# Kernel optimization log

Hardware: AMD Instinct MI355X
Metric: run time of the kernel (lower is better)

Reference implementation:

```python
import jax, jax.numpy as jnp
import numpy as np

B, S, H = 16, 512, 768
T, HD = 9, 64  # num_entity_types, head_size
MASK_VAL = 1e12


def setup_inputs() -> dict:
    key = jax.random.key(0)
    k1, k2 = jax.random.split(key)
    hidden_states = jax.random.normal(k1, (B, S, H), dtype=jnp.float32)
    attention_mask = jnp.ones((B, S), dtype=jnp.int32)
    W_dense = jax.random.normal(k2, (H, T * HD * 2), dtype=jnp.float32) * (H ** -0.5)
    b_dense = jnp.zeros((T * HD * 2,), dtype=jnp.float32)
    return {"hidden_states": hidden_states, "attention_mask": attention_mask,
            "W_dense": W_dense, "b_dense": b_dense}


def _rope_rotate(x, cos_pos, sin_pos):
    # x: [B, S, T, HD]; rotate interleaved pairs
    x2 = jnp.stack([-x[..., 1::2], x[..., ::2]], axis=-1).reshape(x.shape)
    return x * cos_pos + x2 * sin_pos


def reference(hidden_states, attention_mask, W_dense, b_dense):
    b, s, _ = hidden_states.shape
    out = hidden_states @ W_dense + b_dense              # [B,S,T*HD*2]
    out = out.reshape(b, s, T, HD, 2)
    qw, kw = out[..., 0], out[..., 1]                    # [B,S,T,HD]

    # sinusoidal RoPE angles
    pos = jnp.arange(s, dtype=jnp.float32)               # [S]
    inv_freq = jnp.power(10000.0, -2.0 * jnp.arange(HD // 2, dtype=jnp.float32) / HD)
    ang = pos[:, None] * inv_freq[None, :]               # [S, HD/2]
    cos_pos = jnp.repeat(jnp.cos(ang), 2, axis=-1)[None, :, None, :]  # [1,S,1,HD]
    sin_pos = jnp.repeat(jnp.sin(ang), 2, axis=-1)[None, :, None, :]

    qw = _rope_rotate(qw, cos_pos, sin_pos)
    kw = _rope_rotate(kw, cos_pos, sin_pos)

    # biaffine scores: [B,T,S,S]
    logits = jnp.einsum('bmtd,bntd->btmn', qw, kw) / (HD ** 0.5)

    am = attention_mask.astype(logits.dtype)
    pad_mask = (am[:, :, None] * am[:, None, :])[:, None, :, :]  # [B,1,S,S]
    logits = logits - (1.0 - pad_mask) * MASK_VAL

    triu = jnp.triu(jnp.ones((s, s), dtype=logits.dtype), k=0)
    logits = logits - (1.0 - triu) * MASK_VAL
    return logits
```

## Files before the change

### kernel.cpp

```cpp
#include <hip/hip_runtime.h>

#define B_  16
#define S_  512
#define H_  768
#define T_  9
#define HD_ 64
#define N1  (T_*HD_*2)
#define M1  (B_*S_)
#define NT1 (H_/32)

typedef __attribute__((ext_vector_type(8))) short bf16x8;
typedef __attribute__((ext_vector_type(4))) float f32x4;

#define GLB(p) ((const __attribute__((address_space(1))) void*)(p))
#define LDSP(p) ((__attribute__((address_space(3))) void*)(p))

__device__ inline unsigned short f2bf(float f){
  union { float f; unsigned u; } v; v.f = f;
  unsigned r = v.u + 0x7fffu + ((v.u >> 16) & 1u);
  return (unsigned short)(r >> 16);
}

__global__ __launch_bounds__(256) void prep_all(
    const float* __restrict__ hs, short* __restrict__ Abf,
    const float* __restrict__ W, short* __restrict__ Wt,
    float2* __restrict__ tab)
{
  __shared__ float tile[32][33];
  const int bx = blockIdx.x, tid = threadIdx.x;
  if(bx < 3072){
    int i = bx*2048 + tid*8;
    float4 a0 = *(const float4*)(hs + i);
    float4 a1 = *(const float4*)(hs + i + 4);
    bf16x8 r;
    r[0]=f2bf(a0.x); r[1]=f2bf(a0.y); r[2]=f2bf(a0.z); r[3]=f2bf(a0.w);
    r[4]=f2bf(a1.x); r[5]=f2bf(a1.y); r[6]=f2bf(a1.z); r[7]=f2bf(a1.w);
    *(bf16x8*)(Abf + i) = r;
  } else if(bx < 3936){
    int idx = bx - 3072;
    int n0 = (idx % 36)*32, k0 = (idx / 36)*32;
    int tx = tid & 31, ty = tid >> 5;
    #pragma unroll
    for(int r = 0; r < 32; r += 8)
      tile[ty + r][tx] = W[(size_t)(k0 + ty + r)*N1 + n0 + tx];
    __syncthreads();
    #pragma unroll
    for(int r = 0; r < 32; r += 8)
      Wt[(size_t)(n0 + ty + r)*H_ + k0 + tx] = f2bf(tile[tx][ty + r]);
  } else {
    int i = (bx - 3936)*256 + tid;
    int s = i >> 5, p = i & 31;
    float inv = powf(10000.f, -2.f*(float)p/64.f);
    float a = (float)s * inv;
    tab[i] = make_float2(cosf(a), sinf(a));
  }
}

__global__ __launch_bounds__(256) void gemm1_rope(
    const short* __restrict__ Abf, const short* __restrict__ Wt,
    const float* __restrict__ bias, const float2* __restrict__ tab,
    short* __restrict__ Qr, short* __restrict__ Kr)
{
  __shared__ short As[2][128*32];
  __shared__ short Bs[2][128*32];
  const int tid  = threadIdx.x;
  const int lane = tid & 63, w = tid >> 6;
  const int wm = (w >> 1) * 64, wn = (w & 1) * 64;
  const int m0 = blockIdx.x * 128, n0 = blockIdx.y * 128;
  const int lr = lane & 15, lk = (lane >> 4) * 8;

  const int sr = tid >> 2;
  const int sc = (tid & 3) * 8;
  const short* aS = Abf + (size_t)(m0 + sr) * H_ + sc;
  const short* bS = Wt  + (size_t)(n0 + sr) * H_ + sc;
  const int dOff = tid * 8;

#define STAGE1(buf, k0) do{ \
    __builtin_amdgcn_global_load_lds(GLB(aS + (k0)),         LDSP(&As[buf][dOff]),        16, 0, 0); \
    __builtin_amdgcn_global_load_lds(GLB(aS + 64*H_ + (k0)), LDSP(&As[buf][dOff + 2048]), 16, 0, 0); \
    __builtin_amdgcn_global_load_lds(GLB(bS + (k0)),         LDSP(&Bs[buf][dOff]),        16, 0, 0); \
    __builtin_amdgcn_global_load_lds(GLB(bS + 64*H_ + (k0)), LDSP(&Bs[buf][dOff + 2048]), 16, 0, 0); \
  }while(0)

  f32x4 acc[4][4] = {};
  STAGE1(0, 0);

  for(int it = 0; it < NT1; ++it){
    __syncthreads();
    const int cur = it & 1;
    if(it + 1 < NT1) STAGE1(cur ^ 1, (it + 1) * 32);

    bf16x8 aF[4], bF[4];
    #pragma unroll
    for(int i = 0; i < 4; ++i) aF[i] = *(const bf16x8*)(&As[cur][(wm + i*16 + lr)*32 + lk]);
    #pragma unroll
    for(int j = 0; j < 4; ++j) bF[j] = *(const bf16x8*)(&Bs[cur][(wn + j*16 + lr)*32 + lk]);
    #pragma unroll
    for(int i = 0; i < 4; ++i)
      #pragma unroll
      for(int j = 0; j < 4; ++j)
        acc[i][j] = __builtin_amdgcn_mfma_f32_16x16x32_bf16(bF[j], aF[i], acc[i][j], 0, 0, 0);
  }

  const int t = n0 >> 7;
  #pragma unroll
  for(int i = 0; i < 4; ++i){
    int m  = m0 + wm + i*16 + lr;
    int bi = m >> 9, sp = m & 511;
    size_t rowoff = ((size_t)(bi*T_ + t)*S_ + sp)*HD_;
    #pragma unroll
    for(int j = 0; j < 4; ++j){
      int nq  = n0 + wn + j*16 + ((lane >> 4) << 2);
      int hd0 = (nq >> 1) & 63;
      int p   = (nq >> 2) & 31;
      float4 bv = *(const float4*)(bias + nq);
      float2 cs = tab[sp*32 + p];
      float q0 = acc[i][j][0] + bv.x;
      float k0v= acc[i][j][1] + bv.y;
      float q1 = acc[i][j][2] + bv.z;
      float k1v= acc[i][j][3] + bv.w;
      float rq0 = q0*cs.x - q1*cs.y, rq1 = q1*cs.x + q0*cs.y;
      float rk0 = k0v*cs.x - k1v*cs.y, rk1 = k1v*cs.x + k0v*cs.y;
      unsigned uq = (unsigned)f2bf(rq0) | ((unsigned)f2bf(rq1) << 16);
      unsigned uk = (unsigned)f2bf(rk0) | ((unsigned)f2bf(rk1) << 16);
      *(unsigned*)(Qr + rowoff + hd0) = uq;
      *(unsigned*)(Kr + rowoff + hd0) = uk;
    }
  }
}

__global__ __launch_bounds__(256) void gemm2_mask(
    const short* __restrict__ Qr, const short* __restrict__ Kr,
    const int* __restrict__ am, float* __restrict__ out)
{
  const int lane = threadIdx.x & 63;
  const int w    = threadIdx.x >> 6;
  const int bt   = blockIdx.z;
  const int b    = bt / T_;
  const int n0   = blockIdx.x * 128 + (w & 1) * 64;
  const int m0   = blockIdx.y * 128 + (w >> 1) * 64;
  const int lr   = lane & 15;
  const int lk   = (lane >> 4) * 8;

  const short* Q = Qr + (size_t)bt * S_ * HD_;
  const short* K = Kr + (size_t)bt * S_ * HD_;
  f32x4 acc[4][4] = {};

  #pragma unroll
  for(int ks = 0; ks < HD_; ks += 32){
    bf16x8 aF[4], bF[4];
    #pragma unroll
    for(int i = 0; i < 4; ++i) aF[i] = *(const bf16x8*)(Q + (size_t)(m0 + i*16 + lr)*HD_ + ks + lk);
    #pragma unroll
    for(int j = 0; j < 4; ++j) bF[j] = *(const bf16x8*)(K + (size_t)(n0 + j*16 + lr)*HD_ + ks + lk);
    #pragma unroll
    for(int i = 0; i < 4; ++i)
      #pragma unroll
      for(int j = 0; j < 4; ++j)
        acc[i][j] = __builtin_amdgcn_mfma_f32_16x16x32_bf16(bF[j], aF[i], acc[i][j], 0, 0, 0);
  }

  const int* amb = am + b * S_;
  #pragma unroll
  for(int i = 0; i < 4; ++i){
    int m = m0 + i*16 + lr;
    float amm = (float)amb[m];
    float* orow = out + ((size_t)bt*S_ + m)*S_;
    #pragma unroll
    for(int j = 0; j < 4; ++j){
      int nq = n0 + j*16 + ((lane >> 4) << 2);
      int4 a4 = *(const int4*)(amb + nq);
      float4 r;
      r.x = acc[i][j][0]*0.125f - (1.f - amm*(float)a4.x)*1e12f - ((nq+0) < m ? 1e12f : 0.f);
      r.y = acc[i][j][1]*0.125f - (1.f - amm*(float)a4.y)*1e12f - ((nq+1) < m ? 1e12f : 0.f);
      r.z = acc[i][j][2]*0.125f - (1.f - amm*(float)a4.z)*1e12f - ((nq+2) < m ? 1e12f : 0.f);
      r.w = acc[i][j][3]*0.125f - (1.f - amm*(float)a4.w)*1e12f - ((nq+3) < m ? 1e12f : 0.f);
      *(float4*)(orow + nq) = r;
    }
  }
}

extern "C" void kernel_launch(void* const* d_in, const int* in_sizes, int n_in,
                              void* d_out, int out_size, void* d_ws, size_t ws_size,
                              hipStream_t stream)
{
  const float* hs    = (const float*)d_in[0];
  const int*   amask = (const int*)  d_in[1];
  const float* W     = (const float*)d_in[2];
  const float* bias  = (const float*)d_in[3];
  float* out = (float*)d_out;

  char* ws = (char*)d_ws;
  short*  Wt  = (short*) (ws);
  float2* tab = (float2*)(ws + 1769472);
  short*  Qr  = (short*) (ws + 1900544);
  short*  Kr  = (short*) (ws + 11337728);
  short*  Abf = (short*) (ws + 20774912);

  prep_all <<<4000, 256, 0, stream>>>(hs, Abf, W, Wt, tab);
  gemm1_rope<<<dim3(M1/128, N1/128), 256, 0, stream>>>(Abf, Wt, bias, tab, Qr, Kr);
  gemm2_mask<<<dim3(S_/128, S_/128, B_*T_), 256, 0, stream>>>(Qr, Kr, amask, out);
}
```

Baseline: 97.95 us.

## Fuse fp32-to-bf16 activation conversion into GEMM1 A-tile staging

```diff
diff --git a/kernel.cpp b/kernel.cpp
--- a/kernel.cpp
+++ b/kernel.cpp
@@ -21,24 +21,13 @@
   return (unsigned short)(r >> 16);
 }
 
-__global__ __launch_bounds__(256) void prep_all(
-    const float* __restrict__ hs, short* __restrict__ Abf,
-    const float* __restrict__ W, short* __restrict__ Wt,
-    float2* __restrict__ tab)
+__global__ __launch_bounds__(256) void prep_wt(
+    const float* __restrict__ W, short* __restrict__ Wt, float2* __restrict__ tab)
 {
   __shared__ float tile[32][33];
   const int bx = blockIdx.x, tid = threadIdx.x;
-  if(bx < 3072){
-    int i = bx*2048 + tid*8;
-    float4 a0 = *(const float4*)(hs + i);
-    float4 a1 = *(const float4*)(hs + i + 4);
-    bf16x8 r;
-    r[0]=f2bf(a0.x); r[1]=f2bf(a0.y); r[2]=f2bf(a0.z); r[3]=f2bf(a0.w);
-    r[4]=f2bf(a1.x); r[5]=f2bf(a1.y); r[6]=f2bf(a1.z); r[7]=f2bf(a1.w);
-    *(bf16x8*)(Abf + i) = r;
-  } else if(bx < 3936){
-    int idx = bx - 3072;
-    int n0 = (idx % 36)*32, k0 = (idx / 36)*32;
+  if(bx < 864){
+    int n0 = (bx % 36)*32, k0 = (bx / 36)*32;
     int tx = tid & 31, ty = tid >> 5;
     #pragma unroll
     for(int r = 0; r < 32; r += 8)
@@ -46,9 +35,9 @@
     __syncthreads();
     #pragma unroll
     for(int r = 0; r < 32; r += 8)
-      Wt[(size_t)(n0 + ty + r)*H_ + k0 + tx] = f2bf(tile[tx][ty + r]);
+      Wt[(size_t)(n0 + ty + r)*H_ + k0 + tx] = (short)f2bf(tile[tx][ty + r]);
   } else {
-    int i = (bx - 3936)*256 + tid;
+    int i = (bx - 864)*256 + tid;
     int s = i >> 5, p = i & 31;
     float inv = powf(10000.f, -2.f*(float)p/64.f);
     float a = (float)s * inv;
@@ -56,55 +45,84 @@
   }
 }
 
-__global__ __launch_bounds__(256) void gemm1_rope(
-    const short* __restrict__ Abf, const short* __restrict__ Wt,
+__global__ __launch_bounds__(256, 4) void gemm1_rope(
+    const float* __restrict__ hs, const short* __restrict__ Wt,
     const float* __restrict__ bias, const float2* __restrict__ tab,
     short* __restrict__ Qr, short* __restrict__ Kr)
 {
-  __shared__ short As[2][128*32];
+  __shared__ short As[2][64*32];
   __shared__ short Bs[2][128*32];
   const int tid  = threadIdx.x;
   const int lane = tid & 63, w = tid >> 6;
-  const int wm = (w >> 1) * 64, wn = (w & 1) * 64;
-  const int m0 = blockIdx.x * 128, n0 = blockIdx.y * 128;
+  const int wm = (w & 1) * 32, wn = (w >> 1) * 64;
+  const int m0 = blockIdx.x * 64, n0 = blockIdx.y * 128;
   const int lr = lane & 15, lk = (lane >> 4) * 8;
 
-  const int sr = tid >> 2;
-  const int sc = (tid & 3) * 8;
-  const short* aS = Abf + (size_t)(m0 + sr) * H_ + sc;
-  const short* bS = Wt  + (size_t)(n0 + sr) * H_ + sc;
+  const int ar = tid >> 2, ac = (tid & 3) * 8;
+  const float* aS = hs + (size_t)(m0 + ar) * H_ + ac;
+  const short* bS = Wt + (size_t)(n0 + ar) * H_ + ac;
   const int dOff = tid * 8;
 
-#define STAGE1(buf, k0) do{ \
-    __builtin_amdgcn_global_load_lds(GLB(aS + (k0)),         LDSP(&As[buf][dOff]),        16, 0, 0); \
-    __builtin_amdgcn_global_load_lds(GLB(aS + 64*H_ + (k0)), LDSP(&As[buf][dOff + 2048]), 16, 0, 0); \
-    __builtin_amdgcn_global_load_lds(GLB(bS + (k0)),         LDSP(&Bs[buf][dOff]),        16, 0, 0); \
-    __builtin_amdgcn_global_load_lds(GLB(bS + 64*H_ + (k0)), LDSP(&Bs[buf][dOff + 2048]), 16, 0, 0); \
+  f32x4 acc[2][4] = {};
+  float4 ra0, ra1;
+
+#define CVT_DSWRITE(buf) do{ \
+    bf16x8 t_; \
+    t_[0]=f2bf(ra0.x); t_[1]=f2bf(ra0.y); t_[2]=f2bf(ra0.z); t_[3]=f2bf(ra0.w); \
+    t_[4]=f2bf(ra1.x); t_[5]=f2bf(ra1.y); t_[6]=f2bf(ra1.z); t_[7]=f2bf(ra1.w); \
+    *(bf16x8*)(&As[buf][dOff]) = t_; \
   }while(0)
 
-  f32x4 acc[4][4] = {};
-  STAGE1(0, 0);
-
-  for(int it = 0; it < NT1; ++it){
-    __syncthreads();
-    const int cur = it & 1;
-    if(it + 1 < NT1) STAGE1(cur ^ 1, (it + 1) * 32);
-
-    bf16x8 aF[4], bF[4];
-    #pragma unroll
-    for(int i = 0; i < 4; ++i) aF[i] = *(const bf16x8*)(&As[cur][(wm + i*16 + lr)*32 + lk]);
+#define STAGE_B(buf, k0) do{ \
+    __builtin_amdgcn_global_load_lds(GLB(bS + (k0)),          LDSP(&Bs[buf][dOff]),        16, 0, 0); \
+    __builtin_amdgcn_global_load_lds(GLB(bS + 64*H_ + (k0)),  LDSP(&Bs[buf][2048 + dOff]), 16, 0, 0); \
+  }while(0)
+
+  ra0 = *(const float4*)(aS);  ra1 = *(const float4*)(aS + 4);
+  CVT_DSWRITE(0);
+  STAGE_B(0, 0);
+  __builtin_amdgcn_sched_barrier(0);
+  ra0 = *(const float4*)(aS + 32);  ra1 = *(const float4*)(aS + 36);
+  __builtin_amdgcn_sched_barrier(0);
+  asm volatile("s_waitcnt vmcnt(2)" ::: "memory");
+  asm volatile("s_waitcnt lgkmcnt(0)" ::: "memory");
+  __builtin_amdgcn_s_barrier();
+
+  for(int k = 0; k < NT1; ++k){
+    const int cur = k & 1, nxt = cur ^ 1;
+    if(k + 1 < NT1){
+      CVT_DSWRITE(nxt);
+      STAGE_B(nxt, (k + 1) * 32);
+    }
+    __builtin_amdgcn_sched_barrier(0);
+    if(k + 2 < NT1){
+      ra0 = *(const float4*)(aS + (k + 2) * 32);
+      ra1 = *(const float4*)(aS + (k + 2) * 32 + 4);
+    }
+    __builtin_amdgcn_sched_barrier(0);
+
+    bf16x8 aF[2], bF[4];
+    #pragma unroll
+    for(int i = 0; i < 2; ++i) aF[i] = *(const bf16x8*)(&As[cur][(wm + i*16 + lr)*32 + lk]);
     #pragma unroll
     for(int j = 0; j < 4; ++j) bF[j] = *(const bf16x8*)(&Bs[cur][(wn + j*16 + lr)*32 + lk]);
     #pragma unroll
-    for(int i = 0; i < 4; ++i)
+    for(int i = 0; i < 2; ++i)
       #pragma unroll
       for(int j = 0; j < 4; ++j)
         acc[i][j] = __builtin_amdgcn_mfma_f32_16x16x32_bf16(bF[j], aF[i], acc[i][j], 0, 0, 0);
+
+    if(k + 1 < NT1){
+      if(k + 2 < NT1) asm volatile("s_waitcnt vmcnt(2)" ::: "memory");
+      else            asm volatile("s_waitcnt vmcnt(0)" ::: "memory");
+      asm volatile("s_waitcnt lgkmcnt(0)" ::: "memory");
+      __builtin_amdgcn_s_barrier();
+    }
   }
 
   const int t = n0 >> 7;
   #pragma unroll
-  for(int i = 0; i < 4; ++i){
+  for(int i = 0; i < 2; ++i){
     int m  = m0 + wm + i*16 + lr;
     int bi = m >> 9, sp = m & 511;
     size_t rowoff = ((size_t)(bi*T_ + t)*S_ + sp)*HD_;
@@ -127,6 +145,8 @@
       *(unsigned*)(Kr + rowoff + hd0) = uk;
     }
   }
+#undef CVT_DSWRITE
+#undef STAGE_B
 }
 
 __global__ __launch_bounds__(256) void gemm2_mask(
@@ -195,9 +215,8 @@
   float2* tab = (float2*)(ws + 1769472);
   short*  Qr  = (short*) (ws + 1900544);
   short*  Kr  = (short*) (ws + 11337728);
-  short*  Abf = (short*) (ws + 20774912);
-
-  prep_all <<<4000, 256, 0, stream>>>(hs, Abf, W, Wt, tab);
-  gemm1_rope<<<dim3(M1/128, N1/128), 256, 0, stream>>>(Abf, Wt, bias, tab, Qr, Kr);
+
+  prep_wt  <<<928, 256, 0, stream>>>(W, Wt, tab);
+  gemm1_rope<<<dim3(M1/64, N1/128), 256, 0, stream>>>(hs, Wt, bias, tab, Qr, Kr);
   gemm2_mask<<<dim3(S_/128, S_/128, B_*T_), 256, 0, stream>>>(Qr, Kr, amask, out);
 }
```

New measurement: 94.42 us. 3.6% less time.

## Widen GEMM1 K-tile to 64 with XOR-swizzled LDS layout and N-major grid

Applied to the files above, without the earlier changes.

```diff
diff --git a/kernel.cpp b/kernel.cpp
--- a/kernel.cpp
+++ b/kernel.cpp
@@ -7,7 +7,7 @@
 #define HD_ 64
 #define N1  (T_*HD_*2)
 #define M1  (B_*S_)
-#define NT1 (H_/32)
+#define NT1 (H_/64)
 
 typedef __attribute__((ext_vector_type(8))) short bf16x8;
 typedef __attribute__((ext_vector_type(4))) float f32x4;
@@ -21,6 +21,7 @@
   return (unsigned short)(r >> 16);
 }
 
+
 __global__ __launch_bounds__(256) void prep_all(
     const float* __restrict__ hs, short* __restrict__ Abf,
     const float* __restrict__ W, short* __restrict__ Wt,
@@ -30,12 +31,14 @@
   const int bx = blockIdx.x, tid = threadIdx.x;
   if(bx < 3072){
     int i = bx*2048 + tid*8;
+    int row = i / H_, k = i % H_;
     float4 a0 = *(const float4*)(hs + i);
     float4 a1 = *(const float4*)(hs + i + 4);
     bf16x8 r;
     r[0]=f2bf(a0.x); r[1]=f2bf(a0.y); r[2]=f2bf(a0.z); r[3]=f2bf(a0.w);
     r[4]=f2bf(a1.x); r[5]=f2bf(a1.y); r[6]=f2bf(a1.z); r[7]=f2bf(a1.w);
-    *(bf16x8*)(Abf + i) = r;
+    int kk = (k & ~63) | ((k ^ ((row & 7) << 3)) & 63);
+    *(bf16x8*)(Abf + (size_t)row*H_ + kk) = r;
   } else if(bx < 3936){
     int idx = bx - 3072;
     int n0 = (idx % 36)*32, k0 = (idx / 36)*32;
@@ -45,8 +48,11 @@
       tile[ty + r][tx] = W[(size_t)(k0 + ty + r)*N1 + n0 + tx];
     __syncthreads();
     #pragma unroll
-    for(int r = 0; r < 32; r += 8)
-      Wt[(size_t)(n0 + ty + r)*H_ + k0 + tx] = f2bf(tile[tx][ty + r]);
+    for(int r = 0; r < 32; r += 8){
+      int n = n0 + ty + r, k = k0 + tx;
+      int kk = (k & ~63) | ((k ^ ((n & 7) << 3)) & 63);
+      Wt[(size_t)n*H_ + kk] = (short)f2bf(tile[tx][ty + r]);
+    }
   } else {
     int i = (bx - 3936)*256 + tid;
     int s = i >> 5, p = i & 31;
@@ -56,53 +62,62 @@
   }
 }
 
-__global__ __launch_bounds__(256) void gemm1_rope(
+__global__ __launch_bounds__(256, 2) void gemm1_rope(
     const short* __restrict__ Abf, const short* __restrict__ Wt,
     const float* __restrict__ bias, const float2* __restrict__ tab,
     short* __restrict__ Qr, short* __restrict__ Kr)
 {
-  __shared__ short As[2][128*32];
-  __shared__ short Bs[2][128*32];
+  __shared__ short As[2][128*64];
+  __shared__ short Bs[2][128*64];
   const int tid  = threadIdx.x;
   const int lane = tid & 63, w = tid >> 6;
+  const int lr = lane & 15, h = lane >> 4;
   const int wm = (w >> 1) * 64, wn = (w & 1) * 64;
-  const int m0 = blockIdx.x * 128, n0 = blockIdx.y * 128;
-  const int lr = lane & 15, lk = (lane >> 4) * 8;
-
-  const int sr = tid >> 2;
-  const int sc = (tid & 3) * 8;
-  const short* aS = Abf + (size_t)(m0 + sr) * H_ + sc;
-  const short* bS = Wt  + (size_t)(n0 + sr) * H_ + sc;
+  const int n0 = blockIdx.x * 128;
+  const int m0 = blockIdx.y * 128;
+  const int sw = (lr & 7) << 3;
+
+  const short* aS = Abf + (size_t)(m0 + (tid >> 3)) * H_ + (tid & 7) * 8;
+  const short* bS = Wt  + (size_t)(n0 + (tid >> 3)) * H_ + (tid & 7) * 8;
   const int dOff = tid * 8;
 
-#define STAGE1(buf, k0) do{ \
-    __builtin_amdgcn_global_load_lds(GLB(aS + (k0)),         LDSP(&As[buf][dOff]),        16, 0, 0); \
-    __builtin_amdgcn_global_load_lds(GLB(aS + 64*H_ + (k0)), LDSP(&As[buf][dOff + 2048]), 16, 0, 0); \
-    __builtin_amdgcn_global_load_lds(GLB(bS + (k0)),         LDSP(&Bs[buf][dOff]),        16, 0, 0); \
-    __builtin_amdgcn_global_load_lds(GLB(bS + 64*H_ + (k0)), LDSP(&Bs[buf][dOff + 2048]), 16, 0, 0); \
+#define STAGE(buf, k0) do{ \
+    _Pragma("unroll") \
+    for(int q = 0; q < 4; ++q){ \
+      __builtin_amdgcn_global_load_lds(GLB(aS + (size_t)q*32*H_ + (k0)), \
+                                       LDSP(&As[buf][q*2048 + dOff]), 16, 0, 0); \
+      __builtin_amdgcn_global_load_lds(GLB(bS + (size_t)q*32*H_ + (k0)), \
+                                       LDSP(&Bs[buf][q*2048 + dOff]), 16, 0, 0); \
+    } \
   }while(0)
 
   f32x4 acc[4][4] = {};
-  STAGE1(0, 0);
+  STAGE(0, 0);
 
   for(int it = 0; it < NT1; ++it){
     __syncthreads();
     const int cur = it & 1;
-    if(it + 1 < NT1) STAGE1(cur ^ 1, (it + 1) * 32);
-
-    bf16x8 aF[4], bF[4];
-    #pragma unroll
-    for(int i = 0; i < 4; ++i) aF[i] = *(const bf16x8*)(&As[cur][(wm + i*16 + lr)*32 + lk]);
-    #pragma unroll
-    for(int j = 0; j < 4; ++j) bF[j] = *(const bf16x8*)(&Bs[cur][(wn + j*16 + lr)*32 + lk]);
-    #pragma unroll
-    for(int i = 0; i < 4; ++i)
+    if(it + 1 < NT1) STAGE(cur ^ 1, (it + 1) * 64);
+
+    #pragma unroll
+    for(int ks = 0; ks < 2; ++ks){
+      const int kb = ks * 32;
+      bf16x8 aF[4], bF[4];
+      #pragma unroll
+      for(int i = 0; i < 4; ++i)
+        aF[i] = *(const bf16x8*)(&As[cur][(wm + i*16 + lr)*64 + ((kb + h*8) ^ sw)]);
       #pragma unroll
       for(int j = 0; j < 4; ++j)
-        acc[i][j] = __builtin_amdgcn_mfma_f32_16x16x32_bf16(bF[j], aF[i], acc[i][j], 0, 0, 0);
-  }
-
-  const int t = n0 >> 7;
+        bF[j] = *(const bf16x8*)(&Bs[cur][(wn + j*16 + lr)*64 + ((kb + h*8) ^ sw)]);
+      #pragma unroll
+      for(int i = 0; i < 4; ++i)
+        #pragma unroll
+        for(int j = 0; j < 4; ++j)
+          acc[i][j] = __builtin_amdgcn_mfma_f32_16x16x32_bf16(bF[j], aF[i], acc[i][j], 0, 0, 0);
+    }
+  }
+
+  const int t = blockIdx.x;
   #pragma unroll
   for(int i = 0; i < 4; ++i){
     int m  = m0 + wm + i*16 + lr;
@@ -110,7 +125,7 @@
     size_t rowoff = ((size_t)(bi*T_ + t)*S_ + sp)*HD_;
     #pragma unroll
     for(int j = 0; j < 4; ++j){
-      int nq  = n0 + wn + j*16 + ((lane >> 4) << 2);
+      int nq  = n0 + wn + j*16 + (h << 2);
       int hd0 = (nq >> 1) & 63;
       int p   = (nq >> 2) & 31;
       float4 bv = *(const float4*)(bias + nq);
@@ -127,6 +142,7 @@
       *(unsigned*)(Kr + rowoff + hd0) = uk;
     }
   }
+#undef STAGE
 }
 
 __global__ __launch_bounds__(256) void gemm2_mask(
@@ -197,7 +213,7 @@
   short*  Kr  = (short*) (ws + 11337728);
   short*  Abf = (short*) (ws + 20774912);
 
-  prep_all <<<4000, 256, 0, stream>>>(hs, Abf, W, Wt, tab);
-  gemm1_rope<<<dim3(M1/128, N1/128), 256, 0, stream>>>(Abf, Wt, bias, tab, Qr, Kr);
+  prep_all  <<<4000, 256, 0, stream>>>(hs, Abf, W, Wt, tab);
+  gemm1_rope<<<dim3(N1/128, M1/128), 256, 0, stream>>>(Abf, Wt, bias, tab, Qr, Kr);
   gemm2_mask<<<dim3(S_/128, S_/128, B_*T_), 256, 0, stream>>>(Qr, Kr, amask, out);
 }
```

Result: no change. 98.43 us (+0.5%).

## Triple-buffer GEMM1 LDS pipeline, skip masked lower tiles, swizzle GEMM2 grid

Applied to the files above, without the earlier changes.

```diff
diff --git a/kernel.cpp b/kernel.cpp
--- a/kernel.cpp
+++ b/kernel.cpp
@@ -46,7 +46,7 @@
     __syncthreads();
     #pragma unroll
     for(int r = 0; r < 32; r += 8)
-      Wt[(size_t)(n0 + ty + r)*H_ + k0 + tx] = f2bf(tile[tx][ty + r]);
+      Wt[(size_t)(n0 + ty + r)*H_ + k0 + tx] = (short)f2bf(tile[tx][ty + r]);
   } else {
     int i = (bx - 3936)*256 + tid;
     int s = i >> 5, p = i & 31;
@@ -56,26 +56,26 @@
   }
 }
 
-__global__ __launch_bounds__(256) void gemm1_rope(
+__global__ __launch_bounds__(256, 3) void gemm1_rope(
     const short* __restrict__ Abf, const short* __restrict__ Wt,
     const float* __restrict__ bias, const float2* __restrict__ tab,
     short* __restrict__ Qr, short* __restrict__ Kr)
 {
-  __shared__ short As[2][128*32];
-  __shared__ short Bs[2][128*32];
+  __shared__ short As[3][4096];
+  __shared__ short Bs[3][4096];
   const int tid  = threadIdx.x;
   const int lane = tid & 63, w = tid >> 6;
+  const int lr = lane & 15, h = lane >> 4;
+  const int lk = h * 8;
   const int wm = (w >> 1) * 64, wn = (w & 1) * 64;
-  const int m0 = blockIdx.x * 128, n0 = blockIdx.y * 128;
-  const int lr = lane & 15, lk = (lane >> 4) * 8;
-
-  const int sr = tid >> 2;
-  const int sc = (tid & 3) * 8;
-  const short* aS = Abf + (size_t)(m0 + sr) * H_ + sc;
-  const short* bS = Wt  + (size_t)(n0 + sr) * H_ + sc;
+  const int m0 = blockIdx.x * 128;
+  const int n0 = blockIdx.y * 128;
+
+  const short* aS = Abf + (size_t)(m0 + (tid >> 2)) * H_ + (tid & 3) * 8;
+  const short* bS = Wt  + (size_t)(n0 + (tid >> 2)) * H_ + (tid & 3) * 8;
   const int dOff = tid * 8;
 
-#define STAGE1(buf, k0) do{ \
+#define STAGE(buf, k0) do{ \
     __builtin_amdgcn_global_load_lds(GLB(aS + (k0)),         LDSP(&As[buf][dOff]),        16, 0, 0); \
     __builtin_amdgcn_global_load_lds(GLB(aS + 64*H_ + (k0)), LDSP(&As[buf][dOff + 2048]), 16, 0, 0); \
     __builtin_amdgcn_global_load_lds(GLB(bS + (k0)),         LDSP(&Bs[buf][dOff]),        16, 0, 0); \
@@ -83,12 +83,17 @@
   }while(0)
 
   f32x4 acc[4][4] = {};
-  STAGE1(0, 0);
-
+
+  STAGE(0, 0);
+  STAGE(1, 32);
+  asm volatile("s_waitcnt vmcnt(4)\n\ts_barrier" ::: "memory");
+
+  int cur = 0;
   for(int it = 0; it < NT1; ++it){
-    __syncthreads();
-    const int cur = it & 1;
-    if(it + 1 < NT1) STAGE1(cur ^ 1, (it + 1) * 32);
+    if(it + 2 < NT1){
+      const int nb = (cur + 2 >= 3) ? cur - 1 : cur + 2;
+      STAGE(nb, (it + 2) * 32);
+    }
 
     bf16x8 aF[4], bF[4];
     #pragma unroll
@@ -100,9 +105,14 @@
       #pragma unroll
       for(int j = 0; j < 4; ++j)
         acc[i][j] = __builtin_amdgcn_mfma_f32_16x16x32_bf16(bF[j], aF[i], acc[i][j], 0, 0, 0);
-  }
-
-  const int t = n0 >> 7;
+
+    if(it + 3 < NT1)       asm volatile("s_waitcnt vmcnt(4)\n\ts_barrier" ::: "memory");
+    else if(it + 2 < NT1)  asm volatile("s_waitcnt vmcnt(4)\n\ts_barrier" ::: "memory");
+    else if(it + 1 < NT1)  asm volatile("s_waitcnt vmcnt(0)\n\ts_barrier" ::: "memory");
+    cur = (cur + 1 >= 3) ? 0 : cur + 1;
+  }
+
+  const int t = blockIdx.y;
   #pragma unroll
   for(int i = 0; i < 4; ++i){
     int m  = m0 + wm + i*16 + lr;
@@ -110,7 +120,7 @@
     size_t rowoff = ((size_t)(bi*T_ + t)*S_ + sp)*HD_;
     #pragma unroll
     for(int j = 0; j < 4; ++j){
-      int nq  = n0 + wn + j*16 + ((lane >> 4) << 2);
+      int nq  = n0 + wn + j*16 + (h << 2);
       int hd0 = (nq >> 1) & 63;
       int p   = (nq >> 2) & 31;
       float4 bv = *(const float4*)(bias + nq);
@@ -127,6 +137,7 @@
       *(unsigned*)(Kr + rowoff + hd0) = uk;
     }
   }
+#undef STAGE
 }
 
 __global__ __launch_bounds__(256) void gemm2_mask(
@@ -135,12 +146,37 @@
 {
   const int lane = threadIdx.x & 63;
   const int w    = threadIdx.x >> 6;
-  const int bt   = blockIdx.z;
+  const int wg   = ((blockIdx.x & 7) * 288) + (blockIdx.x >> 3);
+  const int bt   = wg >> 4;
+  const int tile = wg & 15;
+  const int mt   = tile >> 2, nt = tile & 3;
   const int b    = bt / T_;
-  const int n0   = blockIdx.x * 128 + (w & 1) * 64;
-  const int m0   = blockIdx.y * 128 + (w >> 1) * 64;
+  const int n0   = nt * 128 + (w & 1) * 64;
+  const int m0   = mt * 128 + (w >> 1) * 64;
   const int lr   = lane & 15;
   const int lk   = (lane >> 4) * 8;
+  const int* amb = am + b * S_;
+
+  if(mt > nt){
+    #pragma unroll
+    for(int i = 0; i < 4; ++i){
+      int m = m0 + i*16 + lr;
+      float amm = (float)amb[m];
+      float* orow = out + ((size_t)bt*S_ + m)*S_;
+      #pragma unroll
+      for(int j = 0; j < 4; ++j){
+        int nq = n0 + j*16 + ((lane >> 4) << 2);
+        int4 a4 = *(const int4*)(amb + nq);
+        float4 r;
+        r.x = -(1.f - amm*(float)a4.x)*1e12f - 1e12f;
+        r.y = -(1.f - amm*(float)a4.y)*1e12f - 1e12f;
+        r.z = -(1.f - amm*(float)a4.z)*1e12f - 1e12f;
+        r.w = -(1.f - amm*(float)a4.w)*1e12f - 1e12f;
+        *(float4*)(orow + nq) = r;
+      }
+    }
+    return;
+  }
 
   const short* Q = Qr + (size_t)bt * S_ * HD_;
   const short* K = Kr + (size_t)bt * S_ * HD_;
@@ -160,7 +196,7 @@
         acc[i][j] = __builtin_amdgcn_mfma_f32_16x16x32_bf16(bF[j], aF[i], acc[i][j], 0, 0, 0);
   }
 
-  const int* amb = am + b * S_;
+  const bool diag = (mt == nt);
   #pragma unroll
   for(int i = 0; i < 4; ++i){
     int m = m0 + i*16 + lr;
@@ -171,10 +207,16 @@
       int nq = n0 + j*16 + ((lane >> 4) << 2);
       int4 a4 = *(const int4*)(amb + nq);
       float4 r;
-      r.x = acc[i][j][0]*0.125f - (1.f - amm*(float)a4.x)*1e12f - ((nq+0) < m ? 1e12f : 0.f);
-      r.y = acc[i][j][1]*0.125f - (1.f - amm*(float)a4.y)*1e12f - ((nq+1) < m ? 1e12f : 0.f);
-      r.z = acc[i][j][2]*0.125f - (1.f - amm*(float)a4.z)*1e12f - ((nq+2) < m ? 1e12f : 0.f);
-      r.w = acc[i][j][3]*0.125f - (1.f - amm*(float)a4.w)*1e12f - ((nq+3) < m ? 1e12f : 0.f);
+      r.x = acc[i][j][0]*0.125f - (1.f - amm*(float)a4.x)*1e12f;
+      r.y = acc[i][j][1]*0.125f - (1.f - amm*(float)a4.y)*1e12f;
+      r.z = acc[i][j][2]*0.125f - (1.f - amm*(float)a4.z)*1e12f;
+      r.w = acc[i][j][3]*0.125f - (1.f - amm*(float)a4.w)*1e12f;
+      if(diag){
+        if((nq+0) < m) r.x -= 1e12f;
+        if((nq+1) < m) r.y -= 1e12f;
+        if((nq+2) < m) r.z -= 1e12f;
+        if((nq+3) < m) r.w -= 1e12f;
+      }
       *(float4*)(orow + nq) = r;
     }
   }
@@ -197,7 +239,7 @@
   short*  Kr  = (short*) (ws + 11337728);
   short*  Abf = (short*) (ws + 20774912);
 
-  prep_all <<<4000, 256, 0, stream>>>(hs, Abf, W, Wt, tab);
+  prep_all  <<<4000, 256, 0, stream>>>(hs, Abf, W, Wt, tab);
   gemm1_rope<<<dim3(M1/128, N1/128), 256, 0, stream>>>(Abf, Wt, bias, tab, Qr, Kr);
-  gemm2_mask<<<dim3(S_/128, S_/128, B_*T_), 256, 0, stream>>>(Qr, Kr, amask, out);
-}
+  gemm2_mask<<<2304, 256, 0, stream>>>(Qr, Kr, amask, out);
+}
```

Measured after the change: 84.16 us. -14.1%, faster.
